# Kernel tuning notes

Measured on AMD Instinct MI355X. Metric: run time of the kernel, lower is better.

## Reference

```python
import jax, jax.numpy as jnp
import numpy as np

IN_C = 1
BASE_C = 16
N3, N2, N1 = 262144, 65536, 16384

def _quadconv(feat, neigh, w, b):
    # feat: [N, C]; neigh: [N, 9] with -1 padding -> gather via extra zero row
    N = feat.shape[0]
    feat_p = jnp.concatenate([feat, jnp.zeros((1, feat.shape[1]), feat.dtype)], axis=0)
    gidx = jnp.where(neigh == -1, N, neigh)
    col = feat_p[gidx].reshape(N, -1)  # [N, 9*C] im2col
    return col @ w.T + b

def _parent_idx(keys, parent_keys):
    return jnp.searchsorted(parent_keys, keys >> 2)

def _quadpool(feat, keys, parent_keys):
    pidx = _parent_idx(keys, parent_keys)
    p = jax.ops.segment_max(feat, pidx, num_segments=parent_keys.shape[0])
    # original inits with -1e9 and zeroes untouched slots; segment_max uses -inf fill
    return jnp.where(jnp.isneginf(p), jnp.zeros((), feat.dtype), p), pidx

def _quadunpool(feat, keys, parent_keys):
    return feat[_parent_idx(keys, parent_keys)]

def _lin(key, out_f, in_f, scale=0.05):
    kw, kb = jax.random.split(key)
    return (jax.random.normal(kw, (out_f, in_f), jnp.float32) * scale,
            jnp.zeros((out_f,), jnp.float32))

def setup_inputs() -> dict:
    key = jax.random.key(0)
    ks = jax.random.split(key, 12)
    inp = {
        'features': jax.random.normal(ks[0], (N3, IN_C), jnp.float32),
        'keys3': jnp.arange(N3, dtype=jnp.int32),
        'keys2': jnp.arange(N2, dtype=jnp.int32),
        'keys1': jnp.arange(N1, dtype=jnp.int32),
        'neighs3': jax.random.randint(ks[1], (N3, 9), -1, N3, jnp.int32),
        'neighs2': jax.random.randint(ks[2], (N2, 9), -1, N2, jnp.int32),
        'neighs1': jax.random.randint(ks[3], (N1, 9), -1, N1, jnp.int32),
    }
    c = BASE_C
    inp['w_enc1'], inp['b_enc1'] = _lin(ks[4], c, 9 * IN_C)
    inp['w_enc2'], inp['b_enc2'] = _lin(ks[5], 2 * c, 9 * c)
    inp['w_enc3'], inp['b_enc3'] = _lin(ks[6], 4 * c, 9 * 2 * c)
    inp['w_dec1'], inp['b_dec1'] = _lin(ks[7], 2 * c, 9 * 4 * c)
    inp['w_dec2'], inp['b_dec2'] = _lin(ks[8], c, 9 * 2 * c)
    inp['w_head'], inp['b_head'] = _lin(ks[9], IN_C, 9 * c)
    return inp

def reference(features, keys3, keys2, keys1, neighs3, neighs2, neighs1,
              w_enc1, b_enc1, w_enc2, b_enc2, w_enc3, b_enc3,
              w_dec1, b_dec1, w_dec2, b_dec2, w_head, b_head):
    relu = jax.nn.relu
    x8 = relu(_quadconv(features, neighs3, w_enc1, b_enc1))
    x7_p, _ = _quadpool(x8, keys3, keys2)
    x7 = relu(_quadconv(x7_p, neighs2, w_enc2, b_enc2))
    x6_p, _ = _quadpool(x7, keys2, keys1)
    x6 = relu(_quadconv(x6_p, neighs1, w_enc3, b_enc3))
    x7_up = _quadunpool(x6, keys2, keys1)
    x7_dec = relu(_quadconv(x7_up, neighs2, w_dec1, b_dec1))
    x8_up = _quadunpool(x7_dec, keys3, keys2)
    x8_dec = relu(_quadconv(x8_up, neighs3, w_dec2, b_dec2))
    return _quadconv(x8_dec, neighs3, w_head, b_head)
```

## Files before the change

kernel.cpp:

```cpp
#include <hip/hip_runtime.h>
#include <stdint.h>

#define NN3 262144
#define NN2 65536
#define NN1 16384

typedef __attribute__((ext_vector_type(8))) __bf16 bf16x8;
typedef __attribute__((ext_vector_type(4))) float floatx4;
typedef __attribute__((ext_vector_type(4))) unsigned int uintx4;

static __device__ __forceinline__ float bf2f(unsigned short u) {
    union { unsigned int i; float f; } v; v.i = ((unsigned int)u) << 16; return v.f;
}
static __device__ __forceinline__ unsigned short f2bf(float f) {
    union { float f; unsigned int i; } v; v.f = f;
    unsigned int x = v.i;
    return (unsigned short)((x + 0x7fffu + ((x >> 16) & 1u)) >> 16);
}
static __device__ __forceinline__ bf16x8 zero_bf16x8() {
    bf16x8 z;
#pragma unroll
    for (int i = 0; i < 8; ++i) z[i] = (__bf16)0.0f;
    return z;
}

template <int CIN, int COUT>
static __device__ __forceinline__ void prep_swz(const float* __restrict__ w,
                                                unsigned short* __restrict__ out, int g) {
    constexpr int K = 9 * CIN, KT = (K + 31) / 32;
    int n = g / (KT * 512);
    int r = g - n * (KT * 512);
    int kt = r >> 9;
    int q = r & 511;
    int lane = q >> 3, e = q & 7;
    int m = lane & 15, quad = lane >> 4;
    int k = kt * 32 + quad * 8 + e;
    float v = (k < K) ? w[(n * 16 + m) * K + k] : 0.0f;
    __builtin_nontemporal_store(f2bf(v), &out[g]);
}

__global__ __launch_bounds__(256) void enc1pool_kernel(
    const float* __restrict__ feat, const int* __restrict__ neigh,
    const float* __restrict__ w, const float* __restrict__ b,
    unsigned short* __restrict__ x7p,
    const float* __restrict__ w_enc2, const float* __restrict__ w_enc3,
    const float* __restrict__ w_dec1, const float* __restrict__ w_dec2,
    unsigned short* __restrict__ wb_enc2, unsigned short* __restrict__ wb_enc3,
    unsigned short* __restrict__ wb_dec1, unsigned short* __restrict__ wb_dec2)
{
    {
        int g = blockIdx.x * 256 + threadIdx.x;
        if (g < 5120) prep_swz<16, 32>(w_enc2, wb_enc2, g);
        else {
            g -= 5120;
            if (g < 18432) prep_swz<32, 64>(w_enc3, wb_enc3, g);
            else {
                g -= 18432;
                if (g < 18432) prep_swz<64, 32>(w_dec1, wb_dec1, g);
                else { g -= 18432; if (g < 4608) prep_swz<32, 16>(w_dec2, wb_dec2, g); }
            }
        }
    }
    __shared__ float ws[144];
    __shared__ float bs[16];
    __shared__ int nsh[2304];
    int t = threadIdx.x;
    if (t < 144) ws[t] = w[t];
    if (t < 16)  bs[t] = b[t];
    int base = blockIdx.x * 256;
    for (int e = t; e < 2304; e += 256)
        nsh[e] = __builtin_nontemporal_load(&neigh[(size_t)base * 9 + e]);
    __syncthreads();
    float f[9];
#pragma unroll
    for (int k = 0; k < 9; ++k) { int j = nsh[t * 9 + k]; f[k] = (j < 0) ? 0.0f : feat[j]; }
    float v[16];
#pragma unroll
    for (int co = 0; co < 16; ++co) {
        float a = bs[co];
#pragma unroll
        for (int k = 0; k < 9; ++k) a += f[k] * ws[co * 9 + k];
        v[co] = fmaxf(a, 0.0f);
    }
#pragma unroll
    for (int co = 0; co < 16; ++co) {
        v[co] = fmaxf(v[co], __shfl_xor(v[co], 1));
        v[co] = fmaxf(v[co], __shfl_xor(v[co], 2));
    }
    if ((t & 3) == 0) {
        unsigned int ov[8];
#pragma unroll
        for (int h = 0; h < 8; ++h)
            ov[h] = (unsigned int)f2bf(v[2 * h]) | (((unsigned int)f2bf(v[2 * h + 1])) << 16);
        uintx4* dst = (uintx4*)(x7p + (size_t)((base + t) >> 2) * 16);
        uintx4 o0 = {ov[0], ov[1], ov[2], ov[3]};
        uintx4 o1 = {ov[4], ov[5], ov[6], ov[7]};
        __builtin_nontemporal_store(o0, dst);
        __builtin_nontemporal_store(o1, dst + 1);
    }
}

template <int CIN, int COUT, bool SHIFT, bool POOL, int TILES, int WN>
__global__ __launch_bounds__(256) void conv_mfma(
    const unsigned short* __restrict__ src, const int* __restrict__ neigh,
    const unsigned short* __restrict__ wb, const float* __restrict__ bias,
    unsigned short* __restrict__ dst)
{
    constexpr int K   = 9 * CIN;
    constexpr int KT  = (K + 31) / 32;
    constexpr int NT  = COUT / 16;
    constexpr int WM  = 4 / WN;
    constexpr int NTW = NT / WN;
    constexpr int ROWS = WM * TILES * 16;
    __shared__ int nsh[ROWS * 9];
    int t = threadIdx.x;
    int rowbase = blockIdx.x * ROWS;
    for (int e = t; e < ROWS * 9; e += 256) {
        int j = __builtin_nontemporal_load(&neigh[(size_t)rowbase * 9 + e]);
        if (SHIFT) j = (j < 0) ? -1 : (j >> 2);
        nsh[e] = j;
    }
    __syncthreads();
    int lane = t & 63;
    int wave = t >> 6;
    int wm   = wave / WN;
    int wn   = wave - wm * WN;
    int m    = lane & 15;
    int quad = lane >> 4;
    int rbase9[TILES];
#pragma unroll
    for (int tl = 0; tl < TILES; ++tl)
        rbase9[tl] = ((wm * TILES + tl) * 16 + m) * 9;

    floatx4 acc[TILES][NTW];
#pragma unroll
    for (int tl = 0; tl < TILES; ++tl)
#pragma unroll
        for (int n = 0; n < NTW; ++n) acc[tl][n] = (floatx4){0.f, 0.f, 0.f, 0.f};

    auto gatherA = [&](int kt, bf16x8 (&dstA)[TILES]) {
        int k0 = kt * 32 + quad * 8;
#pragma unroll
        for (int tl = 0; tl < TILES; ++tl) {
            dstA[tl] = zero_bf16x8();
            if (k0 < K) {
                int j = nsh[rbase9[tl] + k0 / CIN];
                if (j >= 0) dstA[tl] = *(const bf16x8*)(src + (size_t)j * CIN + (k0 % CIN));
            }
        }
    };

    bf16x8 aC[TILES], aP[TILES];
    gatherA(0, aC);
#pragma unroll
    for (int kt = 0; kt < KT; ++kt) {
        if (kt + 1 < KT) gatherA(kt + 1, aP);
#pragma unroll
        for (int n = 0; n < NTW; ++n) {
            int ng = wn * NTW + n;
            bf16x8 bfrag = *(const bf16x8*)(wb + ((size_t)(ng * KT + kt) * 64 + lane) * 8);
#pragma unroll
            for (int tl = 0; tl < TILES; ++tl)
                acc[tl][n] = __builtin_amdgcn_mfma_f32_16x16x32_bf16(aC[tl], bfrag, acc[tl][n], 0, 0, 0);
        }
#pragma unroll
        for (int tl = 0; tl < TILES; ++tl) aC[tl] = aP[tl];
    }

#pragma unroll
    for (int tl = 0; tl < TILES; ++tl) {
        int rg = wm * TILES + tl;
        if (POOL) {
            int p = (rowbase >> 2) + rg * 4 + quad;
#pragma unroll
            for (int n = 0; n < NTW; ++n) {
                int cout = (wn * NTW + n) * 16 + m;
                float vm = fmaxf(fmaxf(acc[tl][n][0], acc[tl][n][1]), fmaxf(acc[tl][n][2], acc[tl][n][3]));
                float v  = fmaxf(vm + bias[cout], 0.0f);
                __builtin_nontemporal_store(f2bf(v), &dst[(size_t)p * COUT + cout]);
            }
        } else {
            int grow = rowbase + rg * 16 + quad * 4;
#pragma unroll
            for (int n = 0; n < NTW; ++n) {
                int cout = (wn * NTW + n) * 16 + m;
                float bv = bias[cout];
#pragma unroll
                for (int r = 0; r < 4; ++r) {
                    float v = fmaxf(acc[tl][n][r] + bv, 0.0f);
                    __builtin_nontemporal_store(f2bf(v), &dst[(size_t)(grow + r) * COUT + cout]);
                }
            }
        }
    }
}

static __device__ __forceinline__ float dot2(unsigned int u, const float* w) {
    return bf2f((unsigned short)(u & 0xffffu)) * w[0] + bf2f((unsigned short)(u >> 16)) * w[1];
}
__global__ __launch_bounds__(256) void head_kernel(
    const unsigned short* __restrict__ x, const int* __restrict__ neigh,
    const float* __restrict__ w, const float* __restrict__ b, float* __restrict__ out)
{
    __shared__ float ws[144];
    __shared__ int nsh[4608];
    int t = threadIdx.x;
    if (t < 144) ws[t] = w[t];
    int base = blockIdx.x * 512;
    for (int e = t; e < 4608; e += 256)
        nsh[e] = __builtin_nontemporal_load(&neigh[(size_t)base * 9 + e]);
    __syncthreads();
    float acc0 = b[0], acc1 = b[0];
#pragma unroll
    for (int k = 0; k < 9; ++k) {
        int j0 = nsh[t * 9 + k];
        int j1 = nsh[(256 + t) * 9 + k];
        const float* wp = &ws[k * 16];
        if (j0 >= 0) {
            const uint4* r = (const uint4*)(x + (size_t)j0 * 16);
            uint4 r0 = r[0], r1 = r[1];
            acc0 += dot2(r0.x, wp)     + dot2(r0.y, wp + 2)  + dot2(r0.z, wp + 4)  + dot2(r0.w, wp + 6);
            acc0 += dot2(r1.x, wp + 8) + dot2(r1.y, wp + 10) + dot2(r1.z, wp + 12) + dot2(r1.w, wp + 14);
        }
        if (j1 >= 0) {
            const uint4* r = (const uint4*)(x + (size_t)j1 * 16);
            uint4 r0 = r[0], r1 = r[1];
            acc1 += dot2(r0.x, wp)     + dot2(r0.y, wp + 2)  + dot2(r0.z, wp + 4)  + dot2(r0.w, wp + 6);
            acc1 += dot2(r1.x, wp + 8) + dot2(r1.y, wp + 10) + dot2(r1.z, wp + 12) + dot2(r1.w, wp + 14);
        }
    }
    __builtin_nontemporal_store(acc0, &out[base + t]);
    __builtin_nontemporal_store(acc1, &out[base + 256 + t]);
}

extern "C" void kernel_launch(void* const* d_in, const int* in_sizes, int n_in,
                              void* d_out, int out_size, void* d_ws, size_t ws_size,
                              hipStream_t stream) {
    const float* features = (const float*)d_in[0];
    const int* neighs3 = (const int*)d_in[4];
    const int* neighs2 = (const int*)d_in[5];
    const int* neighs1 = (const int*)d_in[6];
    const float* w_enc1 = (const float*)d_in[7];
    const float* b_enc1 = (const float*)d_in[8];
    const float* w_enc2 = (const float*)d_in[9];
    const float* b_enc2 = (const float*)d_in[10];
    const float* w_enc3 = (const float*)d_in[11];
    const float* b_enc3 = (const float*)d_in[12];
    const float* w_dec1 = (const float*)d_in[13];
    const float* b_dec1 = (const float*)d_in[14];
    const float* w_dec2 = (const float*)d_in[15];
    const float* b_dec2 = (const float*)d_in[16];
    const float* w_head = (const float*)d_in[17];
    const float* b_head = (const float*)d_in[18];

    char* ws = (char*)d_ws;
    size_t off = 0;
    unsigned short* wb_enc2 = (unsigned short*)(ws + off); off += 5120 * 2;
    unsigned short* wb_enc3 = (unsigned short*)(ws + off); off += 18432 * 2;
    unsigned short* wb_dec1 = (unsigned short*)(ws + off); off += 18432 * 2;
    unsigned short* wb_dec2 = (unsigned short*)(ws + off); off += 4608 * 2;
    unsigned short* x7p   = (unsigned short*)(ws + off); off += (size_t)NN2 * 16 * 2;
    unsigned short* x6p   = (unsigned short*)(ws + off); off += (size_t)NN1 * 32 * 2;
    unsigned short* x6    = (unsigned short*)(ws + off); off += (size_t)NN1 * 64 * 2;
    unsigned short* x7dec = (unsigned short*)(ws + off); off += (size_t)NN2 * 32 * 2;
    unsigned short* x8dec = (unsigned short*)(ws + off); off += (size_t)NN3 * 16 * 2;

    enc1pool_kernel<<<NN3 / 256, 256, 0, stream>>>(features, neighs3, w_enc1, b_enc1, x7p,
                                                   w_enc2, w_enc3, w_dec1, w_dec2,
                                                   wb_enc2, wb_enc3, wb_dec1, wb_dec2);
    conv_mfma<16, 32, false, true, 2, 2><<<NN2 / 64, 256, 0, stream>>>(x7p, neighs2, wb_enc2, b_enc2, x6p);
    conv_mfma<32, 64, false, false, 1, 4><<<NN1 / 16, 256, 0, stream>>>(x6p, neighs1, wb_enc3, b_enc3, x6);
    conv_mfma<64, 32, true, false, 2, 2><<<NN2 / 64, 256, 0, stream>>>(x6, neighs2, wb_dec1, b_dec1, x7dec);
    conv_mfma<32, 16, true, false, 4, 1><<<NN3 / 256, 256, 0, stream>>>(x7dec, neighs3, wb_dec2, b_dec2, x8dec);
    head_kernel<<<NN3 / 512, 256, 0, stream>>>(x8dec, neighs3, w_head, b_head, (float*)d_out);
}
```

Baseline: 204.6 us.

## Deepen gather prefetch ring in MFMA convs and head, drop nontemporal stores

The MFMA conv kernels replace the double-buffered neighbour gather with a four-deep register ring, so more gather loads are in flight while the MFMAs run. The head kernel now handles one row per thread with a four-deep prefetch of neighbour rows, and launches twice as many blocks. Intermediate outputs written with nontemporal stores become ordinary stores, so they stay in cache for the next layer to read. Costs are more registers per thread, which may lower occupancy, and the lost ILP from the head kernel's former two rows per thread.

```diff
diff --git a/kernel.cpp b/kernel.cpp
--- a/kernel.cpp
+++ b/kernel.cpp
@@ -36,7 +36,7 @@
     int m = lane & 15, quad = lane >> 4;
     int k = kt * 32 + quad * 8 + e;
     float v = (k < K) ? w[(n * 16 + m) * K + k] : 0.0f;
-    __builtin_nontemporal_store(f2bf(v), &out[g]);
+    out[g] = f2bf(v);
 }
 
 __global__ __launch_bounds__(256) void enc1pool_kernel(
@@ -95,8 +95,8 @@
         uintx4* dst = (uintx4*)(x7p + (size_t)((base + t) >> 2) * 16);
         uintx4 o0 = {ov[0], ov[1], ov[2], ov[3]};
         uintx4 o1 = {ov[4], ov[5], ov[6], ov[7]};
-        __builtin_nontemporal_store(o0, dst);
-        __builtin_nontemporal_store(o1, dst + 1);
+        dst[0] = o0;
+        dst[1] = o1;
     }
 }
 
@@ -112,6 +112,8 @@
     constexpr int WM  = 4 / WN;
     constexpr int NTW = NT / WN;
     constexpr int ROWS = WM * TILES * 16;
+    constexpr int PF  = 4;
+    static_assert(KT >= PF, "ring deeper than K-loop");
     __shared__ int nsh[ROWS * 9];
     int t = threadIdx.x;
     int rowbase = blockIdx.x * ROWS;
@@ -150,34 +152,34 @@
         }
     };
 
-    bf16x8 aC[TILES], aP[TILES];
-    gatherA(0, aC);
+    bf16x8 aB[PF][TILES];
+#pragma unroll
+    for (int p = 0; p < PF; ++p) gatherA(p, aB[p]);
+
 #pragma unroll
     for (int kt = 0; kt < KT; ++kt) {
-        if (kt + 1 < KT) gatherA(kt + 1, aP);
 #pragma unroll
         for (int n = 0; n < NTW; ++n) {
             int ng = wn * NTW + n;
             bf16x8 bfrag = *(const bf16x8*)(wb + ((size_t)(ng * KT + kt) * 64 + lane) * 8);
 #pragma unroll
             for (int tl = 0; tl < TILES; ++tl)
-                acc[tl][n] = __builtin_amdgcn_mfma_f32_16x16x32_bf16(aC[tl], bfrag, acc[tl][n], 0, 0, 0);
-        }
-#pragma unroll
-        for (int tl = 0; tl < TILES; ++tl) aC[tl] = aP[tl];
+                acc[tl][n] = __builtin_amdgcn_mfma_f32_16x16x32_bf16(aB[kt % PF][tl], bfrag, acc[tl][n], 0, 0, 0);
+        }
+        if (kt + PF < KT) gatherA(kt + PF, aB[kt % PF]);
     }
 
 #pragma unroll
     for (int tl = 0; tl < TILES; ++tl) {
         int rg = wm * TILES + tl;
         if (POOL) {
-            int p = (rowbase >> 2) + rg * 4 + quad;
+            int pp = (rowbase >> 2) + rg * 4 + quad;
 #pragma unroll
             for (int n = 0; n < NTW; ++n) {
                 int cout = (wn * NTW + n) * 16 + m;
                 float vm = fmaxf(fmaxf(acc[tl][n][0], acc[tl][n][1]), fmaxf(acc[tl][n][2], acc[tl][n][3]));
                 float v  = fmaxf(vm + bias[cout], 0.0f);
-                __builtin_nontemporal_store(f2bf(v), &dst[(size_t)p * COUT + cout]);
+                dst[(size_t)pp * COUT + cout] = f2bf(v);
             }
         } else {
             int grow = rowbase + rg * 16 + quad * 4;
@@ -188,7 +190,7 @@
 #pragma unroll
                 for (int r = 0; r < 4; ++r) {
                     float v = fmaxf(acc[tl][n][r] + bv, 0.0f);
-                    __builtin_nontemporal_store(f2bf(v), &dst[(size_t)(grow + r) * COUT + cout]);
+                    dst[(size_t)(grow + r) * COUT + cout] = f2bf(v);
                 }
             }
         }
@@ -203,34 +205,45 @@
     const float* __restrict__ w, const float* __restrict__ b, float* __restrict__ out)
 {
     __shared__ float ws[144];
-    __shared__ int nsh[4608];
+    __shared__ int nsh[2304];
     int t = threadIdx.x;
     if (t < 144) ws[t] = w[t];
-    int base = blockIdx.x * 512;
-    for (int e = t; e < 4608; e += 256)
+    int base = blockIdx.x * 256;
+    for (int e = t; e < 2304; e += 256)
         nsh[e] = __builtin_nontemporal_load(&neigh[(size_t)base * 9 + e]);
     __syncthreads();
-    float acc0 = b[0], acc1 = b[0];
+    int idx[9];
+#pragma unroll
+    for (int k = 0; k < 9; ++k) idx[k] = nsh[t * 9 + k];
+
+    uint4 ra[4], rb[4];
+    const uint4 z4 = make_uint4(0u, 0u, 0u, 0u);
+#pragma unroll
+    for (int p = 0; p < 4; ++p) {
+        ra[p] = z4; rb[p] = z4;
+        int j = idx[p];
+        if (j >= 0) {
+            const uint4* r = (const uint4*)(x + (size_t)j * 16);
+            ra[p] = r[0]; rb[p] = r[1];
+        }
+    }
+    float acc = b[0];
 #pragma unroll
     for (int k = 0; k < 9; ++k) {
-        int j0 = nsh[t * 9 + k];
-        int j1 = nsh[(256 + t) * 9 + k];
         const float* wp = &ws[k * 16];
-        if (j0 >= 0) {
-            const uint4* r = (const uint4*)(x + (size_t)j0 * 16);
-            uint4 r0 = r[0], r1 = r[1];
-            acc0 += dot2(r0.x, wp)     + dot2(r0.y, wp + 2)  + dot2(r0.z, wp + 4)  + dot2(r0.w, wp + 6);
-            acc0 += dot2(r1.x, wp + 8) + dot2(r1.y, wp + 10) + dot2(r1.z, wp + 12) + dot2(r1.w, wp + 14);
-        }
-        if (j1 >= 0) {
-            const uint4* r = (const uint4*)(x + (size_t)j1 * 16);
-            uint4 r0 = r[0], r1 = r[1];
-            acc1 += dot2(r0.x, wp)     + dot2(r0.y, wp + 2)  + dot2(r0.z, wp + 4)  + dot2(r0.w, wp + 6);
-            acc1 += dot2(r1.x, wp + 8) + dot2(r1.y, wp + 10) + dot2(r1.z, wp + 12) + dot2(r1.w, wp + 14);
-        }
-    }
-    __builtin_nontemporal_store(acc0, &out[base + t]);
-    __builtin_nontemporal_store(acc1, &out[base + 256 + t]);
+        uint4 r0 = ra[k & 3], r1 = rb[k & 3];
+        acc += dot2(r0.x, wp)     + dot2(r0.y, wp + 2)  + dot2(r0.z, wp + 4)  + dot2(r0.w, wp + 6);
+        acc += dot2(r1.x, wp + 8) + dot2(r1.y, wp + 10) + dot2(r1.z, wp + 12) + dot2(r1.w, wp + 14);
+        if (k + 4 < 9) {
+            int j = idx[k + 4];
+            ra[k & 3] = z4; rb[k & 3] = z4;
+            if (j >= 0) {
+                const uint4* r = (const uint4*)(x + (size_t)j * 16);
+                ra[k & 3] = r[0]; rb[k & 3] = r[1];
+            }
+        }
+    }
+    out[base + t] = acc;
 }
 
 extern "C" void kernel_launch(void* const* d_in, const int* in_sizes, int n_in,
@@ -272,5 +285,5 @@
     conv_mfma<32, 64, false, false, 1, 4><<<NN1 / 16, 256, 0, stream>>>(x6p, neighs1, wb_enc3, b_enc3, x6);
     conv_mfma<64, 32, true, false, 2, 2><<<NN2 / 64, 256, 0, stream>>>(x6, neighs2, wb_dec1, b_dec1, x7dec);
     conv_mfma<32, 16, true, false, 4, 1><<<NN3 / 256, 256, 0, stream>>>(x7dec, neighs3, wb_dec2, b_dec2, x8dec);
-    head_kernel<<<NN3 / 512, 256, 0, stream>>>(x8dec, neighs3, w_head, b_head, (float*)d_out);
-}
+    head_kernel<<<NN3 / 256, 256, 0, stream>>>(x8dec, neighs3, w_head, b_head, (float*)d_out);
+}
```

New measurement: 202.9 us. No clear change (-0.8%).
